# Performance work log

Hardware: AMD Instinct MI355X
Metric: run time of the kernel (lower is better)

Reference implementation:

```python
import jax, jax.numpy as jnp
import numpy as np

B, H, W = 4, 256, 256
TARGET_BETA0 = 5
TARGET_LIFETIME = 0.5
LOSS_SCALE = 100.0


def setup_inputs() -> dict:
    key = jax.random.key(0)
    k1, k2 = jax.random.split(key)
    prob_map = jax.random.uniform(k1, (B, 1, H, W), dtype=jnp.float32)
    roi_mask = (jax.random.uniform(k2, (B, 1, H, W)) < 0.9).astype(jnp.float32)
    return {"prob_map": prob_map, "roi_mask": roi_mask}


def _ph0_topk_loss(f):
    """0-dim persistent homology (V-filtration, 4-connectivity) of f:[H,W],
    then standard top-k MSE(target_lifetime) loss. Equivalent to
    cripser.compute_ph_torch(f, maxdim=0, filtration='V') + _standard_loss.
    Algorithm: Kruskal over grid edges with weight max(f[u],f[v]), elder rule.
    All combinatorics run on stop_gradient values; births/deaths are
    differentiable gathers from f at the paired pixel indices."""
    Hh, Ww = f.shape
    N = Hh * Ww
    fv = f.reshape(-1)
    fvc = jax.lax.stop_gradient(fv)

    idx2d = jnp.arange(N, dtype=jnp.int32).reshape(Hh, Ww)
    r_u = idx2d[:, :-1].reshape(-1)  # right edges
    r_v = r_u + 1
    d_u = idx2d[:-1, :].reshape(-1)  # down edges
    d_v = d_u + Ww
    eu = jnp.concatenate([r_u, d_u])
    ev = jnp.concatenate([r_v, d_v])
    ew = jnp.maximum(fvc[eu], fvc[ev])
    order = jnp.argsort(ew)  # process edges by increasing filtration value
    eu, ev = eu[order], ev[order]

    parent0 = jnp.arange(N, dtype=jnp.int32)

    def step(parent, uv):
        u, v = uv[0], uv[1]

        def find(x):
            return jax.lax.while_loop(lambda y: parent[y] != y, lambda y: parent[y], x)

        ru = find(u)
        rv = find(v)
        merge = ru != rv
        # Invariant: a root is the argmin pixel of its component, so
        # fvc[root] is the component's birth value. Elder rule: the root
        # with smaller birth value survives (ties -> smaller index).
        older_u = (fvc[ru] < fvc[rv]) | ((fvc[ru] == fvc[rv]) & (ru < rv))
        keep = jnp.where(older_u, ru, rv)
        die = jnp.where(older_u, rv, ru)
        b_idx = jnp.where(merge, die, -1)  # birth pixel of the dying comp
        d_pix = jnp.where(fvc[u] >= fvc[v], u, v)  # death = max endpoint
        d_idx = jnp.where(merge, d_pix, -1)
        parent = parent.at[die].set(jnp.where(merge, keep, die))
        parent = parent.at[u].set(jnp.where(merge, keep, ru))  # path compression
        parent = parent.at[v].set(jnp.where(merge, keep, rv))
        return parent, (b_idx, d_idx)

    _, (pb, pd_) = jax.lax.scan(step, parent0, jnp.stack([eu, ev], axis=1))

    valid = pb >= 0
    births = fv[jnp.maximum(pb, 0)]
    deaths = fv[jnp.maximum(pd_, 0)]
    life = jnp.where(valid, deaths - births, 0.0)  # lifetimes >= 0

    # sort descending; invalid slots to the end (keys are stop-gradient)
    key_ = jnp.where(valid, jax.lax.stop_gradient(life), -jnp.inf)
    top = jnp.argsort(-key_)[:TARGET_BETA0]
    topk = life[top]
    vk = valid[top]
    n_use = jnp.sum(vk)  # = min(num_finite, target_beta0)
    sq = jnp.where(vk, (topk - TARGET_LIFETIME) ** 2, 0.0)
    return jnp.sum(sq) / jnp.maximum(n_use, 1).astype(f.dtype)


def reference(prob_map, roi_mask):
    prob = prob_map[:, 0] * roi_mask[:, 0]  # roi masking; (1-roi)*0 is a no-op
    filtration = 1.0 - prob
    losses = jax.vmap(_ph0_topk_loss)(filtration)
    return jnp.mean(losses) * LOSS_SCALE
```

## Files before the change

### kernel.cpp

```cpp
#include <hip/hip_runtime.h>
#include <stdint.h>

#define NPIX 65536
#define NE   130560
#define NIMG 4
#define LTPB 1024
#define ETPB 1024
#define NBLK_L (NIMG*32)
#define TPIX 2048
#define EPAD 4096
#define KMAX 4096
#define HSZ  1024
#define LHSZ 2048
#define ECAP 4096
#define NCUT 2560
#define MTAILL 256
#define ETAIL  256
typedef unsigned long long u64;

__device__ __forceinline__ int ufind(unsigned* lbl, int x){
  int r = x, c = (int)lbl[r];
  while (c != r){ r = c; c = (int)lbl[r]; }
  while ((int)lbl[x] != r){ int n = (int)lbl[x]; lbl[x] = (unsigned)r; x = n; }
  return r;
}
__device__ __forceinline__ int ufind16(unsigned short* uf, int x){
  int r = x, c = (int)uf[r];
  while (c != r){ r = c; c = (int)uf[r]; }
  while ((int)uf[x] != r){ int n = (int)uf[x]; uf[x] = (unsigned short)r; x = n; }
  return r;
}

__device__ __forceinline__ void merge5(float* a, const float* b){
  float out[5]; int ia = 0, ib = 0;
  #pragma unroll
  for (int k = 0; k < 5; ++k){
    float av = (ia < 5) ? a[ia] : -2.0f;
    float bv = (ib < 5) ? b[ib] : -2.0f;
    if (av >= bv){ out[k] = av; ++ia; } else { out[k] = bv; ++ib; }
  }
  #pragma unroll
  for (int k = 0; k < 5; ++k) a[k] = out[k];
}

__device__ __forceinline__ void ins5(float* t5, float v){
  if (v > t5[4]){
    int j = 4;
    while (j > 0 && t5[j-1] < v){ t5[j] = t5[j-1]; --j; }
    t5[j] = v;
  }
}

__global__ __launch_bounds__(LTPB)
void ph0_local(const float* __restrict__ prob, const float* __restrict__ roi,
               float* __restrict__ LIFEg, unsigned* __restrict__ CIDg,
               u64* __restrict__ LAg,
               unsigned* __restrict__ C, unsigned* __restrict__ C2,
               unsigned* __restrict__ CUTWg, u64* __restrict__ RNKIg,
               float* __restrict__ T5g)
{
  const int blk = blockIdx.x;
  const int img = blk >> 5;
  const int tile = blk & 31;
  const int tr = tile >> 2, tc = tile & 3;
  const int gr0 = tr*32, gc0 = tc*64;
  const int tid = threadIdx.x;
  const int lane = tid & 63;

  const float* pm = prob + img*NPIX;
  const float* rm = roi  + img*NPIX;
  float* LIFE = LIFEg + img*NPIX;
  unsigned* CID = CIDg + img*NPIX;
  unsigned* CUTW = CUTWg + img*NCUT;
  u64* RNKI = RNKIg + (size_t)img*NPIX;
  u64* LA = LAg + (size_t)img*NE;

  __shared__ float          sf[TPIX];
  __shared__ unsigned       slbl[TPIX];
  __shared__ unsigned       smeb[2][TPIX];
  __shared__ float          slife[TPIX];
  __shared__ unsigned       blkm[TPIX];
  __shared__ unsigned short el[2][EPAD];
  __shared__ unsigned       aux[EPAD];
  __shared__ unsigned short fdl[2][EPAD];
  __shared__ unsigned       bkw[192];
  __shared__ unsigned short bkp[192];
  __shared__ unsigned       s_fired[TPIX/32];
  __shared__ float          s_t5w[(LTPB/64)*5];
  __shared__ int s_n[3];
  __shared__ int s_fd[2];

  float t5[5] = {-1.f,-1.f,-1.f,-1.f,-1.f};

  for (int p = tid; p < TPIX; p += LTPB){
    int gp = ((gr0 + (p>>6))<<8) + gc0 + (p&63);
    float fv = 1.0f - pm[gp]*rm[gp];
    sf[p] = fv; slbl[p] = (unsigned)p;
    smeb[0][p] = 0xFFFFFFFFu; smeb[1][p] = 0xFFFFFFFFu;
    blkm[p] = 0xFFFFFFFFu;
    slife[p] = 0.0f;
  }
  if (tid < 3) s_n[tid] = 0;
  if (tid < 2) s_fd[tid] = 0;
  if (tid < TPIX/32) s_fired[tid] = 0;
  for (int s = tid; s < 192; s += LTPB){
    unsigned wv = 0xFFFFFFFFu; int p = 0; int gq = -1;
    if (s < 32){ if (tc > 0){ p = s*64;        gq = ((gr0+s)<<8)    + gc0 - 1;  } }
    else if (s < 64){ int k=s-32;  if (tc < 3){ p = k*64+63;  gq = ((gr0+k)<<8)  + gc0 + 64; } }
    else if (s < 128){ int k=s-64; if (tr > 0){ p = k;        gq = ((gr0-1)<<8)  + gc0 + k;  } }
    else { int k=s-128;            if (tr < 7){ p = 31*64+k;  gq = ((gr0+32)<<8) + gc0 + k;  } }
    if (gq >= 0){
      int gp = ((gr0 + (p>>6))<<8) + gc0 + (p&63);
      float fp = 1.0f - pm[gp]*rm[gp];
      float fq = 1.0f - pm[gq]*rm[gq];
      wv = __float_as_uint(fmaxf(fp, fq));
    }
    bkw[s] = wv; bkp[s] = (unsigned short)p;
  }
  __syncthreads();

  if (tid < 192){
    int s = tid;
    if (s >= 32 && s < 64  && tc < 3) CUTW[(tc<<8) | (gr0 + (s-32))] = bkw[s];
    if (s >= 128           && tr < 7) CUTW[768 + (tr<<8) + (gc0 + (s-128))] = bkw[s];
    if (bkw[s] != 0xFFFFFFFFu) atomicMin(&blkm[(int)bkp[s]], bkw[s]);
  }

  int M = EPAD, cur = 0, rd = 0;
  bool tailm = false;
  for (; rd < 100000; ++rd){
    int nxt = cur ^ 1;
    unsigned* sme  = smeb[rd & 1];
    unsigned* smeN = smeb[(rd+1) & 1];
    {
      int pv = (rd & 1) ^ 1;
      int fc = s_fd[pv];
      for (int i = tid; i < fc; i += LTPB){
        int d = (int)fdl[pv][i];
        atomicMin(&blkm[ufind(slbl, d)], blkm[d]);
      }
    }
    int Mpad = (M + 63) & ~63;
    for (int idx = tid; idx < Mpad; idx += LTPB){
      bool keep = false; int e=0,u=0,v=0,a=0,b=0;
      if (idx < M){
        e = (rd == 0) ? idx : (int)el[cur][idx];
        bool valid;
        if (e < 2048){ u=e; v=e+1; valid = ((e&63)!=63); }
        else { u=e-2048; v=u+64; valid = ((u>>6)!=31); }
        if (valid){
          a = ufind(slbl,u); b = ufind(slbl,v);
          if (a != b){
            unsigned wb = __float_as_uint(fmaxf(sf[u],sf[v]));
            atomicMin(&sme[a],wb); atomicMin(&sme[b],wb);
            keep = true;
          }
        }
      }
      u64 m = __ballot(keep);
      if (m){
        int pos0 = __popcll(m & ((1ULL<<lane)-1));
        int leader = __ffsll((long long)m)-1;
        int base = 0;
        if (lane == leader) base = atomicAdd(&s_n[rd%3], __popcll(m));
        base = __shfl(base, leader);
        if (keep){
          el[nxt][base+pos0] = (unsigned short)e;
          aux[base+pos0] = (unsigned)a | ((unsigned)b<<16);
        }
      }
    }
    __syncthreads();
    int n = s_n[rd%3];
    cur = nxt;
    if (n == M || n == 0){ M = n; break; }
    M = n;
    for (int idx = tid; idx < M; idx += LTPB){
      int e = (int)el[cur][idx];
      unsigned ab = aux[idx];
      int a = (int)(ab & 0xFFFFu), b = (int)(ab >> 16);
      int u, v;
      if (e < 2048){ u = e; v = e + 1; } else { u = e - 2048; v = u + 64; }
      float w = fmaxf(sf[u], sf[v]);
      unsigned wb = __float_as_uint(w);
      float fa = sf[a], fb = sf[b];
      bool bd = (fb < fa) || ((fb == fa) && (b < a));
      int die = bd ? a : b, keep = bd ? b : a;
      bool fire = false;
      if (sme[die] == wb && blkm[die] >= wb){
        fire = true;
        slbl[die] = (unsigned)keep;
        float lt = w - (bd ? fa : fb);
        slife[die] = lt;
        atomicMin(&blkm[keep], blkm[die]);
        unsigned bbit = 1u << (die & 31);
        if (!(atomicOr(&s_fired[die >> 5], bbit) & bbit)) ins5(t5, lt);
      }
      smeN[a] = 0xFFFFFFFFu; smeN[b] = 0xFFFFFFFFu;
      u64 fm = __ballot(fire);
      if (fm){
        int pos0 = __popcll(fm & ((1ULL<<lane)-1));
        int leader = __ffsll((long long)fm)-1;
        int base2 = 0;
        if (lane == leader) base2 = atomicAdd(&s_fd[rd&1], __popcll(fm));
        base2 = __shfl(base2, leader);
        if (fire) fdl[rd&1][base2+pos0] = (unsigned short)die;
      }
    }
    if (tid == 0){ s_n[(rd+1)%3] = 0; s_fd[(rd&1)^1] = 0; }
    __syncthreads();
    if (M <= MTAILL){ ++rd; tailm = true; break; }
  }

  if (tailm){
    if (tid < 64){
      for (;; ++rd){
        unsigned* sme  = smeb[rd & 1];
        unsigned* smeN = smeb[(rd+1) & 1];
        {
          int pv = (rd & 1) ^ 1;
          int fc = s_fd[pv];
          for (int i = lane; i < fc; i += 64){
            int d = (int)fdl[pv][i];
            atomicMin(&blkm[ufind(slbl, d)], blkm[d]);
          }
        }
        __builtin_amdgcn_wave_barrier();
        int nxt = cur ^ 1;
        int nacc = 0;
        for (int i0 = 0; i0 < M; i0 += 64){
          int idx = i0 + lane;
          bool keep = false; int e = 0, a = 0, b = 0;
          if (idx < M){
            e = (int)el[cur][idx];
            int u, v;
            if (e < 2048){ u = e; v = e + 1; } else { u = e - 2048; v = u + 64; }
            a = ufind(slbl,u); b = ufind(slbl,v);
            if (a != b){
              unsigned wb = __float_as_uint(fmaxf(sf[u],sf[v]));
              atomicMin(&sme[a],wb); atomicMin(&sme[b],wb);
              keep = true;
            }
          }
          u64 mm = __ballot(keep);
          if (keep){
            int pos = nacc + __popcll(mm & ((1ULL<<lane)-1));
            el[nxt][pos] = (unsigned short)e;
            aux[pos] = (unsigned)a | ((unsigned)b<<16);
          }
          nacc += __popcll(mm);
        }
        __builtin_amdgcn_wave_barrier();
        int n = nacc;
        cur = nxt;
        if (n == M || n == 0){ M = n; break; }
        M = n;
        int fdc = 0;
        for (int i0 = 0; i0 < M; i0 += 64){
          int idx = i0 + lane;
          bool fire = false; int die = 0;
          if (idx < M){
            int e = (int)el[cur][idx];
            unsigned ab = aux[idx];
            int a = (int)(ab & 0xFFFFu), b = (int)(ab >> 16);
            int u, v;
            if (e < 2048){ u = e; v = e + 1; } else { u = e - 2048; v = u + 64; }
            float w = fmaxf(sf[u], sf[v]);
            unsigned wb = __float_as_uint(w);
            float fa = sf[a], fb = sf[b];
            bool bd = (fb < fa) || ((fb == fa) && (b < a));
            die = bd ? a : b;
            int kp = bd ? b : a;
            if (sme[die] == wb && blkm[die] >= wb){
              fire = true;
              slbl[die] = (unsigned)kp;
              float lt = w - (bd ? fa : fb);
              slife[die] = lt;
              atomicMin(&blkm[kp], blkm[die]);
              unsigned bbit = 1u << (die & 31);
              if (!(atomicOr(&s_fired[die >> 5], bbit) & bbit)) ins5(t5, lt);
            }
            smeN[a] = 0xFFFFFFFFu; smeN[b] = 0xFFFFFFFFu;
          }
          u64 fm = __ballot(fire);
          if (fire){
            int pos = fdc + __popcll(fm & ((1ULL<<lane)-1));
            fdl[rd&1][pos] = (unsigned short)die;
          }
          fdc += __popcll(fm);
        }
        if (lane == 0){ s_fd[rd&1] = fdc; s_fd[(rd&1)^1] = 0; }
        __builtin_amdgcn_wave_barrier();
      }
      if (lane == 0){ s_n[0] = M; s_n[1] = cur; }
    }
    __syncthreads();
    M = s_n[0]; cur = s_n[1];
  }

  unsigned* posm = smeb[0];
  for (int p = tid; p < TPIX; p += LTPB){
    if ((int)slbl[p] == p){
      unsigned pos = atomicAdd(&C2[img], 1u);
      posm[p] = pos;
      unsigned gp = (unsigned)(((gr0 + (p>>6))<<8) + gc0 + (p&63));
      RNKI[pos] = ((u64)__float_as_uint(sf[p]) << 32) | gp;
    }
  }
  __syncthreads();
  for (int p = tid; p < TPIX; p += LTPB){
    int r = ufind(slbl, p);
    int gp = ((gr0 + (p>>6))<<8) + gc0 + (p&63);
    CID[gp] = posm[r];
    LIFE[gp] = slife[p];
  }
  __syncthreads();

  unsigned* hk = (unsigned*)&el[cur ^ 1][0];
  unsigned* hw = slbl;
  for (int i = tid; i < LHSZ; i += LTPB){ hk[i] = 0xFFFFFFFFu; hw[i] = 0xFFFFFFFFu; }
  __syncthreads();

  unsigned* ctr = &C[img];
  int Mpad2 = (M + 63) & ~63;
  for (int idx = tid; idx < Mpad2; idx += LTPB){
    bool spill = false;
    u64 rec = 0;
    if (idx < M){
      int e = (int)el[cur][idx];
      unsigned ab = aux[idx];
      int a = (int)(ab & 0xFFFFu), b = (int)(ab >> 16);
      int u, v;
      if (e < 2048){ u = e; v = e + 1; } else { u = e - 2048; v = u + 64; }
      unsigned wb = __float_as_uint(fmaxf(sf[u], sf[v]));
      int lo = a < b ? a : b, hi = a < b ? b : a;
      unsigned key = ((unsigned)lo << 11) | (unsigned)hi;
      unsigned h = ((key * 2654435761u) >> 21) & (LHSZ-1);
      bool ins = false;
      #pragma unroll
      for (int t = 0; t < 8; ++t){
        unsigned old = atomicCAS(&hk[h], 0xFFFFFFFFu, key);
        if (old == 0xFFFFFFFFu || old == key){ atomicMin(&hw[h], wb); ins = true; break; }
        h = (h + 1) & (LHSZ-1);
      }
      if (!ins){
        spill = true;
        rec = ((u64)wb << 32) | ((u64)posm[a] << 16) | posm[b];
      }
    }
    u64 m = __ballot(spill);
    if (m){
      int pos0 = __popcll(m & ((1ULL<<lane)-1));
      int leader = __ffsll((long long)m)-1;
      unsigned base = 0;
      if (lane == leader) base = atomicAdd(ctr, (unsigned)__popcll(m));
      base = (unsigned)__shfl((int)base, leader);
      if (spill) LA[base + pos0] = rec;
    }
  }
  __syncthreads();
  for (int h = tid; h < LHSZ; h += LTPB){
    unsigned key = hk[h];
    bool ok = (key != 0xFFFFFFFFu);
    u64 rec = 0;
    if (ok){
      int a = (int)(key >> 11), b = (int)(key & 0x7FFu);
      rec = ((u64)hw[h] << 32) | ((u64)posm[a] << 16) | posm[b];
    }
    u64 m = __ballot(ok);
    if (m){
      int pos0 = __popcll(m & ((1ULL<<lane)-1));
      int leader = __ffsll((long long)m)-1;
      unsigned base = 0;
      if (lane == leader) base = atomicAdd(ctr, (unsigned)__popcll(m));
      base = (unsigned)__shfl((int)base, leader);
      if (ok) LA[base + pos0] = rec;
    }
  }

  #pragma unroll
  for (int off = 1; off < 64; off <<= 1){
    float o[5];
    #pragma unroll
    for (int k = 0; k < 5; ++k) o[k] = __shfl_xor(t5[k], off);
    merge5(t5, o);
  }
  if (lane == 0){
    int wv = tid >> 6;
    #pragma unroll
    for (int k = 0; k < 5; ++k) s_t5w[wv*5+k] = t5[k];
  }
  __syncthreads();
  if (tid < 64){
    float u5[5];
    #pragma unroll
    for (int k = 0; k < 5; ++k) u5[k] = (tid < LTPB/64) ? s_t5w[tid*5+k] : -2.0f;
    #pragma unroll
    for (int off = 1; off < 16; off <<= 1){
      float o[5];
      #pragma unroll
      for (int k = 0; k < 5; ++k) o[k] = __shfl_xor(u5[k], off);
      merge5(u5, o);
    }
    if (tid == 0){
      #pragma unroll
      for (int k = 0; k < 5; ++k) T5g[blk*5+k] = u5[k];
    }
  }
}

#define RUN_ROUNDS_GLOBAL(UF, ME, RNK)                                       \
  for (int k = tid; k < K; k += ETPB) UF[k] = (unsigned short)k;             \
  __syncthreads();                                                           \
  for (int rdg = 0; rdg < 70000 && n > 0; ++rdg){                            \
    for (int k = tid; k < K; k += ETPB) ME[k] = 0xFFFFFFFFu;                 \
    if (tid == 0) s_n[0] = 0;                                                \
    __syncthreads();                                                         \
    int Mpad = (n + 63) & ~63;                                               \
    for (int idx = tid; idx < Mpad; idx += ETPB){                            \
      bool keep = false; unsigned wb = 0; int a = 0, b = 0;                  \
      if (idx < n){                                                          \
        u64 rec = src[idx];                                                  \
        wb = (unsigned)(rec >> 32);                                          \
        a = (int)((rec >> 16) & 0xFFFFu);                                    \
        b = (int)(rec & 0xFFFFu);                                            \
        a = ufind16(UF, a); b = ufind16(UF, b);                              \
        if (a != b){ atomicMin(&ME[a], wb); atomicMin(&ME[b], wb); keep = true; } \
      }                                                                      \
      u64 m = __ballot(keep);                                                \
      if (m){                                                                \
        int pos0 = __popcll(m & ((1ULL<<lane)-1));                           \
        int leader = __ffsll((long long)m)-1;                                \
        int base = 0;                                                        \
        if (lane == leader) base = atomicAdd(&s_n[0], __popcll(m));          \
        base = __shfl(base, leader);                                         \
        if (keep) dst[base+pos0] = ((u64)wb<<32)|((u64)(unsigned)a<<16)|(unsigned)b; \
      }                                                                      \
    }                                                                        \
    __syncthreads();                                                         \
    int nn = s_n[0];                                                         \
    for (int idx = tid; idx < nn; idx += ETPB){                              \
      u64 rec = dst[idx];                                                    \
      unsigned wb = (unsigned)(rec >> 32);                                   \
      int a = (int)((rec >> 16) & 0xFFFFu);                                  \
      int b = (int)(rec & 0xFFFFu);                                          \
      bool bd = RNK[b] < RNK[a];                                             \
      int die = bd ? a : b, kp = bd ? b : a;                                 \
      if (ME[die] == wb){                                                    \
        UF[die] = (unsigned short)kp;                                        \
        u64 rk = RNK[die];                                                   \
        life[(unsigned)(rk & 0xFFFFFFFFu)] =                                 \
            __uint_as_float(wb) - __uint_as_float((unsigned)(rk >> 32));     \
      }                                                                      \
    }                                                                        \
    __syncthreads();                                                         \
    u64* t = src; src = dst; dst = t; n = nn;                                \
  }

__global__ __launch_bounds__(ETPB)
void ph0_endgame(float* __restrict__ LIFEg, unsigned* __restrict__ CIDg,
                 const unsigned* __restrict__ CUTWg, u64* __restrict__ RNKIg,
                 u64* __restrict__ LAg, u64* __restrict__ LBg,
                 const unsigned* __restrict__ C, const unsigned* __restrict__ C2,
                 const float* __restrict__ T5g,
                 float* __restrict__ LOSS, unsigned* __restrict__ DONE,
                 float* __restrict__ out)
{
  const int img = blockIdx.x, tid = threadIdx.x;
  const int lane = tid & 63;
  float* life = LIFEg + img*NPIX;
  unsigned* cid = CIDg + img*NPIX;
  const unsigned* cw = CUTWg + img*NCUT;
  u64* RNKI = RNKIg + (size_t)img*NPIX;
  u64* src = LAg + (size_t)img*NE;
  u64* dst = LBg + (size_t)img*NE;

  __shared__ unsigned short s_uf[KMAX];
  __shared__ unsigned s_meB[2*KMAX];
  __shared__ unsigned s_hkB[2*HSZ];
  __shared__ unsigned s_hwB[2*HSZ];
  __shared__ u64 s_rnk[KMAX];
  __shared__ u64 s_lstA[ECAP];
  __shared__ u64 s_lstB[ECAP];
  __shared__ unsigned s_fired[KMAX/32];
  __shared__ float s_w5[(ETPB/64)*5];
  __shared__ int s_n[3];

  const int K = (int)C2[img];
  const int nInt = (int)C[img];

  for (int s = tid; s < NCUT; s += ETPB){
    int gu, gv;
    if (s < 768){ int ci = s >> 8, row = s & 255, col = 63 + (ci<<6); gu = (row<<8)+col; gv = gu+1; }
    else { int k = s - 768; int ri = k >> 8, colh = k & 255, gr = 31 + (ri<<5); gu = (gr<<8)+colh; gv = gu+256; }
    unsigned ia = cid[gu];
    unsigned ib = cid[gv];
    unsigned wb = cw[s];
    s_lstA[s] = ((u64)wb << 32) | ((u64)ia << 16) | ib;
  }
  if (tid < 3) s_n[tid] = 0;
  int n = nInt + NCUT;

  float t5[5] = {-1.f,-1.f,-1.f,-1.f,-1.f};

  if (K <= KMAX){
    for (int k = tid; k < K; k += ETPB){
      s_uf[k] = (unsigned short)k;
      s_rnk[k] = RNKI[k];
      s_meB[k] = 0xFFFFFFFFu;
    }
    for (int h = tid; h < HSZ; h += ETPB){ s_hkB[h] = 0xFFFFFFFFu; s_hwB[h] = 0xFFFFFFFFu; }
    if (tid < KMAX/32) s_fired[tid] = 0;
    if (tid < 32*5) ins5(t5, T5g[img*(32*5) + tid]);
    __syncthreads();

    u64 *lsrc = s_lstA, *ldst = s_lstB;
    int rd = 0; bool tailm = false;

    for (; rd < 70000; ++rd){
      const int bi = rd & 1;
      unsigned* me  = s_meB + bi*KMAX;
      unsigned* meN = s_meB + (bi^1)*KMAX;
      unsigned* hk = s_hkB + bi*HSZ;
      unsigned* hw = s_hwB + bi*HSZ;
      const bool useHash = (n > 1024);
      int Mpad = (n + 63) & ~63;
      for (int idx = tid; idx < Mpad; idx += ETPB){
        bool app = false; unsigned wb = 0; int a = 0, b = 0;
        if (idx < n){
          u64 rec;
          if (rd == 0) rec = (idx < NCUT) ? lsrc[idx] : src[idx - NCUT];
          else         rec = (idx < ECAP) ? lsrc[idx] : src[idx];
          a = (int)((rec >> 16) & 0xFFFFu);
          b = (int)(rec & 0xFFFFu);
          a = ufind16(s_uf, a); b = ufind16(s_uf, b);
          if (a != b){
            wb = (unsigned)(rec >> 32);
            if (useHash){
              int lo = a < b ? a : b, hi = a < b ? b : a;
              unsigned key = ((unsigned)lo << 12) | (unsigned)hi;
              unsigned h = ((key * 2654435761u) >> 20) & (HSZ-1);
              bool ins = false;
              #pragma unroll
              for (int t = 0; t < 8; ++t){
                unsigned old = atomicCAS(&hk[h], 0xFFFFFFFFu, key);
                if (old == 0xFFFFFFFFu || old == key){ atomicMin(&hw[h], wb); ins = true; break; }
                h = (h + 1) & (HSZ-1);
              }
              if (!ins){ atomicMin(&me[a], wb); atomicMin(&me[b], wb); app = true; }
            } else {
              atomicMin(&me[a], wb); atomicMin(&me[b], wb); app = true;
            }
          }
        }
        u64 m = __ballot(app);
        if (m){
          int pos0 = __popcll(m & ((1ULL<<lane)-1));
          int leader = __ffsll((long long)m)-1;
          int base = 0;
          if (lane == leader) base = atomicAdd(&s_n[rd%3], __popcll(m));
          base = __shfl(base, leader);
          if (app){
            u64 r = ((u64)wb<<32)|((u64)(unsigned)a<<16)|(unsigned)b;
            int pos = base+pos0;
            if (pos < ECAP) ldst[pos] = r; else dst[pos] = r;
          }
        }
      }
      __syncthreads();
      if (useHash){
        for (int h = tid; h < HSZ; h += ETPB){
          unsigned key = hk[h];
          bool okk = (key != 0xFFFFFFFFu);
          unsigned wb = 0; int a = 0, b = 0;
          if (okk){
            a = (int)(key >> 12); b = (int)(key & 0xFFFu);
            wb = hw[h];
            atomicMin(&me[a], wb); atomicMin(&me[b], wb);
          }
          u64 m = __ballot(okk);
          if (m){
            int pos0 = __popcll(m & ((1ULL<<lane)-1));
            int leader = __ffsll((long long)m)-1;
            int base = 0;
            if (lane == leader) base = atomicAdd(&s_n[rd%3], __popcll(m));
            base = __shfl(base, leader);
            if (okk){
              u64 r = ((u64)wb<<32)|((u64)(unsigned)a<<16)|(unsigned)b;
              int pos = base+pos0;
              if (pos < ECAP) ldst[pos] = r; else dst[pos] = r;
            }
          }
        }
        __syncthreads();
      }
      int nn = s_n[rd%3];
      if (nn == 0) break;
      for (int idx = tid; idx < nn; idx += ETPB){
        u64 rec = (idx < ECAP) ? ldst[idx] : dst[idx];
        unsigned wb = (unsigned)(rec >> 32);
        int a = (int)((rec >> 16) & 0xFFFFu);
        int b = (int)(rec & 0xFFFFu);
        u64 ra = s_rnk[a], rb = s_rnk[b];
        bool bd = rb < ra;
        int die = bd ? a : b, kp = bd ? b : a;
        if (me[die] == wb){
          s_uf[die] = (unsigned short)kp;
          unsigned bbit = 1u << (die & 31);
          if (!(atomicOr(&s_fired[die >> 5], bbit) & bbit)){
            u64 rk = bd ? ra : rb;
            ins5(t5, __uint_as_float(wb) - __uint_as_float((unsigned)(rk >> 32)));
          }
        }
        meN[a] = 0xFFFFFFFFu; meN[b] = 0xFFFFFFFFu;
      }
      if (nn > 1024){
        unsigned* hkN = s_hkB + (bi^1)*HSZ;
        unsigned* hwN = s_hwB + (bi^1)*HSZ;
        for (int h = tid; h < HSZ; h += ETPB){ hkN[h] = 0xFFFFFFFFu; hwN[h] = 0xFFFFFFFFu; }
      }
      if (tid == 0) s_n[(rd+1)%3] = 0;
      __syncthreads();
      { u64* t = src; src = dst; dst = t; }
      { u64* t2 = lsrc; lsrc = ldst; ldst = t2; }
      n = nn;
      if (n <= ETAIL){ ++rd; tailm = true; break; }
    }

    if (tailm){
      if (tid < 64){
        for (;; ++rd){
          const int bi = rd & 1;
          unsigned* me  = s_meB + bi*KMAX;
          unsigned* meN = s_meB + (bi^1)*KMAX;
          int nacc = 0;
          for (int i0 = 0; i0 < n; i0 += 64){
            int idx = i0 + lane;
            bool app = false; unsigned wb = 0; int a = 0, b = 0;
            if (idx < n){
              u64 rec = lsrc[idx];
              a = (int)((rec >> 16) & 0xFFFFu);
              b = (int)(rec & 0xFFFFu);
              a = ufind16(s_uf, a); b = ufind16(s_uf, b);
              if (a != b){
                wb = (unsigned)(rec >> 32);
                atomicMin(&me[a], wb); atomicMin(&me[b], wb);
                app = true;
              }
            }
            u64 mm = __ballot(app);
            if (app){
              int pos = nacc + __popcll(mm & ((1ULL<<lane)-1));
              ldst[pos] = ((u64)wb<<32)|((u64)(unsigned)a<<16)|(unsigned)b;
            }
            nacc += __popcll(mm);
          }
          __builtin_amdgcn_wave_barrier();
          int nn = nacc;
          if (nn == 0) break;
          for (int i0 = 0; i0 < nn; i0 += 64){
            int idx = i0 + lane;
            if (idx < nn){
              u64 rec = ldst[idx];
              unsigned wb = (unsigned)(rec >> 32);
              int a = (int)((rec >> 16) & 0xFFFFu);
              int b = (int)(rec & 0xFFFFu);
              u64 ra = s_rnk[a], rb = s_rnk[b];
              bool bd = rb < ra;
              int die = bd ? a : b, kp = bd ? b : a;
              if (me[die] == wb){
                s_uf[die] = (unsigned short)kp;
                unsigned bbit = 1u << (die & 31);
                if (!(atomicOr(&s_fired[die >> 5], bbit) & bbit)){
                  u64 rk = bd ? ra : rb;
                  ins5(t5, __uint_as_float(wb) - __uint_as_float((unsigned)(rk >> 32)));
                }
              }
              meN[a] = 0xFFFFFFFFu; meN[b] = 0xFFFFFFFFu;
            }
          }
          __builtin_amdgcn_wave_barrier();
          { u64* t2 = lsrc; lsrc = ldst; ldst = t2; }
          n = nn;
        }
      }
      __syncthreads();
    }
  } else {
    __syncthreads();
    for (int s = tid; s < NCUT; s += ETPB) src[nInt + s] = s_lstA[s];
    __syncthreads();
    unsigned short* g_uf = (unsigned short*)cid;
    unsigned*       g_me = (unsigned*)(cid + NPIX/2);
    u64*            g_rnk = RNKI;
    RUN_ROUNDS_GLOBAL(g_uf, g_me, g_rnk)
    for (int i = tid; i < NPIX; i += ETPB) ins5(t5, life[i]);
  }

  #pragma unroll
  for (int off = 1; off < 64; off <<= 1){
    float o[5];
    #pragma unroll
    for (int k = 0; k < 5; ++k) o[k] = __shfl_xor(t5[k], off);
    merge5(t5, o);
  }
  if (lane == 0){
    int wv = tid >> 6;
    #pragma unroll
    for (int k = 0; k < 5; ++k) s_w5[wv*5+k] = t5[k];
  }
  __syncthreads();
  if (tid < 64){
    float u5[5];
    #pragma unroll
    for (int k = 0; k < 5; ++k) u5[k] = (tid < ETPB/64) ? s_w5[tid*5+k] : -2.0f;
    #pragma unroll
    for (int off = 1; off < 16; off <<= 1){
      float o[5];
      #pragma unroll
      for (int k = 0; k < 5; ++k) o[k] = __shfl_xor(u5[k], off);
      merge5(u5, o);
    }
    if (tid == 0){
      float lsum = 0.0f;
      #pragma unroll
      for (int k = 0; k < 5; ++k){ float d = u5[k] - 0.5f; lsum += d*d; }
      atomicExch(&LOSS[img], lsum * 0.2f);
      __threadfence();
      unsigned prev = atomicAdd(DONE, 1u);
      if (prev == NIMG - 1){
        float s = 0.0f;
        #pragma unroll
        for (int i = 0; i < NIMG; ++i) s += atomicAdd(&LOSS[i], 0.0f);
        out[0] = s * 25.0f;
      }
    }
  }
}

extern "C" void kernel_launch(void* const* d_in, const int* in_sizes, int n_in,
                              void* d_out, int out_size, void* d_ws, size_t ws_size,
                              hipStream_t stream)
{
  const float* prob = (const float*)d_in[0];
  const float* roi  = (const float*)d_in[1];
  char* ws = (char*)d_ws;
  const size_t SZL = (size_t)4*NE*8;
  float*    LIFE = (float*)(ws + (1u<<20));
  unsigned* CID  = (unsigned*)(ws + (2u<<20));
  unsigned* CUTW = (unsigned*)(ws + (3u<<20));
  u64*      LA   = (u64*)(ws + (5u<<20));
  u64*      LB   = (u64*)(ws + (5u<<20) + SZL);
  u64*      RNKI = (u64*)(ws + (5u<<20) + 2*SZL);
  unsigned* C    = (unsigned*)(ws + (5u<<20) + 2*SZL + (2u<<20));
  unsigned* C2   = C + 4;
  unsigned* DONE = C + 8;
  float*    LOSS = (float*)((char*)C + 64);
  float*    T5   = (float*)(ws + (5u<<20) + 2*SZL - 2560);
  float*    out  = (float*)d_out;

  hipMemsetAsync(C, 0, 64, stream);
  ph0_local<<<NBLK_L, LTPB, 0, stream>>>(prob, roi, LIFE, CID, LA, C, C2, CUTW, RNKI, T5);
  ph0_endgame<<<NIMG, ETPB, 0, stream>>>(LIFE, CID, CUTW, RNKI, LA, LB, C, C2, T5, LOSS, DONE, out);
}
```

Baseline: 263.0 us.

## Replace Boruvka tail rounds with bitonic-sorted Kruskal sweep using per-wave claims

```diff
diff --git a/kernel.cpp b/kernel.cpp
--- a/kernel.cpp
+++ b/kernel.cpp
@@ -14,8 +14,9 @@
 #define LHSZ 2048
 #define ECAP 4096
 #define NCUT 2560
-#define MTAILL 256
-#define ETAIL  256
+#define MTAILL 512
+#define ETAIL  512
+#define RCAPL 40
 typedef unsigned long long u64;
 
 __device__ __forceinline__ int ufind(unsigned* lbl, int x){
@@ -209,93 +210,102 @@
     }
     if (tid == 0){ s_n[(rd+1)%3] = 0; s_fd[(rd&1)^1] = 0; }
     __syncthreads();
-    if (M <= MTAILL){ ++rd; tailm = true; break; }
+    if (M <= MTAILL || rd >= RCAPL){ ++rd; tailm = true; break; }
   }
 
   if (tailm){
+    {
+      int pv = (rd & 1) ^ 1;
+      int fc = s_fd[pv];
+      for (int i = tid; i < fc; i += LTPB){
+        int d = (int)fdl[pv][i];
+        atomicMin(&blkm[ufind(slbl, d)], blkm[d]);
+      }
+    }
+    int P = 1; while (P < M) P <<= 1;
+    unsigned* skey = aux;
+    unsigned short* sval = el[cur];
+    unsigned* claim = smeb[0];
+    for (int i = tid; i < P; i += LTPB){
+      if (i < M){
+        int e = (int)sval[i];
+        int u, v;
+        if (e < 2048){ u = e; v = e + 1; } else { u = e - 2048; v = u + 64; }
+        skey[i] = __float_as_uint(fmaxf(sf[u], sf[v]));
+      } else skey[i] = 0xFFFFFFFFu;
+    }
+    for (int i = tid; i < TPIX; i += LTPB) claim[i] = 0xFFFFFFFFu;
+    __syncthreads();
+    for (int k = 2; k <= P; k <<= 1){
+      for (int j = k >> 1; j > 0; j >>= 1){
+        for (int i = tid; i < P; i += LTPB){
+          int l = i ^ j;
+          if (l > i){
+            unsigned ki = skey[i], kl = skey[l];
+            if ((ki > kl) == ((i & k) == 0)){
+              skey[i] = kl; skey[l] = ki;
+              unsigned short tv = sval[i]; sval[i] = sval[l]; sval[l] = tv;
+            }
+          }
+        }
+        __syncthreads();
+      }
+    }
     if (tid < 64){
-      for (;; ++rd){
-        unsigned* sme  = smeb[rd & 1];
-        unsigned* smeN = smeb[(rd+1) & 1];
-        {
-          int pv = (rd & 1) ^ 1;
-          int fc = s_fd[pv];
-          for (int i = lane; i < fc; i += 64){
-            int d = (int)fdl[pv][i];
-            atomicMin(&blkm[ufind(slbl, d)], blkm[d]);
-          }
-        }
-        __builtin_amdgcn_wave_barrier();
-        int nxt = cur ^ 1;
-        int nacc = 0;
-        for (int i0 = 0; i0 < M; i0 += 64){
-          int idx = i0 + lane;
-          bool keep = false; int e = 0, a = 0, b = 0;
-          if (idx < M){
-            e = (int)el[cur][idx];
-            int u, v;
-            if (e < 2048){ u = e; v = e + 1; } else { u = e - 2048; v = u + 64; }
-            a = ufind(slbl,u); b = ufind(slbl,v);
-            if (a != b){
-              unsigned wb = __float_as_uint(fmaxf(sf[u],sf[v]));
-              atomicMin(&sme[a],wb); atomicMin(&sme[b],wb);
-              keep = true;
-            }
-          }
-          u64 mm = __ballot(keep);
-          if (keep){
-            int pos = nacc + __popcll(mm & ((1ULL<<lane)-1));
-            el[nxt][pos] = (unsigned short)e;
-            aux[pos] = (unsigned)a | ((unsigned)b<<16);
-          }
-          nacc += __popcll(mm);
-        }
-        __builtin_amdgcn_wave_barrier();
-        int n = nacc;
-        cur = nxt;
-        if (n == M || n == 0){ M = n; break; }
-        M = n;
-        int fdc = 0;
-        for (int i0 = 0; i0 < M; i0 += 64){
-          int idx = i0 + lane;
-          bool fire = false; int die = 0;
-          if (idx < M){
-            int e = (int)el[cur][idx];
-            unsigned ab = aux[idx];
-            int a = (int)(ab & 0xFFFFu), b = (int)(ab >> 16);
-            int u, v;
-            if (e < 2048){ u = e; v = e + 1; } else { u = e - 2048; v = u + 64; }
-            float w = fmaxf(sf[u], sf[v]);
-            unsigned wb = __float_as_uint(w);
+      int survM = 0;
+      for (int base = 0; base < M; base += 64){
+        int rank = base + lane;
+        bool live = (rank < M), surv = false;
+        int e = 0, u = 0, v = 0; unsigned wb = 0;
+        if (live){
+          e = (int)sval[rank];
+          if (e < 2048){ u = e; v = e + 1; } else { u = e - 2048; v = u + 64; }
+          wb = skey[rank];
+        }
+        for (int si = 0; si < 8192; ++si){
+          if (!__ballot(live)) break;
+          int a = 0, b = 0; bool cl = false;
+          if (live){
+            a = ufind(slbl, u); b = ufind(slbl, v);
+            if (a == b) live = false;
+            else { atomicMin(&claim[a], (unsigned)rank);
+                   atomicMin(&claim[b], (unsigned)rank); cl = true; }
+          }
+          __builtin_amdgcn_wave_barrier();
+          if (live && cl && claim[a] == (unsigned)rank && claim[b] == (unsigned)rank){
             float fa = sf[a], fb = sf[b];
             bool bd = (fb < fa) || ((fb == fa) && (b < a));
-            die = bd ? a : b;
-            int kp = bd ? b : a;
-            if (sme[die] == wb && blkm[die] >= wb){
-              fire = true;
+            int die = bd ? a : b, kp = bd ? b : a;
+            if (blkm[die] < wb){
+              surv = true;
+              atomicMin(&blkm[a], wb);
+              atomicMin(&blkm[b], wb);
+            } else {
               slbl[die] = (unsigned)kp;
-              float lt = w - (bd ? fa : fb);
+              atomicMin(&blkm[kp], blkm[die]);
+              float lt = __uint_as_float(wb) - (bd ? fa : fb);
               slife[die] = lt;
-              atomicMin(&blkm[kp], blkm[die]);
               unsigned bbit = 1u << (die & 31);
               if (!(atomicOr(&s_fired[die >> 5], bbit) & bbit)) ins5(t5, lt);
             }
-            smeN[a] = 0xFFFFFFFFu; smeN[b] = 0xFFFFFFFFu;
-          }
-          u64 fm = __ballot(fire);
-          if (fire){
-            int pos = fdc + __popcll(fm & ((1ULL<<lane)-1));
-            fdl[rd&1][pos] = (unsigned short)die;
-          }
-          fdc += __popcll(fm);
-        }
-        if (lane == 0){ s_fd[rd&1] = fdc; s_fd[(rd&1)^1] = 0; }
-        __builtin_amdgcn_wave_barrier();
-      }
-      if (lane == 0){ s_n[0] = M; s_n[1] = cur; }
+            live = false;
+          }
+          __builtin_amdgcn_wave_barrier();
+          if (cl){ claim[a] = 0xFFFFFFFFu; claim[b] = 0xFFFFFFFFu; }
+          __builtin_amdgcn_wave_barrier();
+        }
+        u64 sm = __ballot(surv);
+        if (surv){
+          int pos = survM + __popcll(sm & ((1ULL << lane) - 1));
+          el[cur ^ 1][pos] = (unsigned short)e;
+        }
+        survM += __popcll(sm);
+      }
+      if (lane == 0) s_n[0] = survM;
     }
     __syncthreads();
-    M = s_n[0]; cur = s_n[1];
+    M = s_n[0];
+    cur ^= 1;
   }
 
   unsigned* posm = smeb[0];
@@ -313,6 +323,13 @@
     int gp = ((gr0 + (p>>6))<<8) + gc0 + (p&63);
     CID[gp] = posm[r];
     LIFE[gp] = slife[p];
+  }
+  __syncthreads();
+  for (int idx = tid; idx < M; idx += LTPB){
+    int e = (int)el[cur][idx];
+    int u, v;
+    if (e < 2048){ u = e; v = e + 1; } else { u = e - 2048; v = u + 64; }
+    aux[idx] = (unsigned)ufind(slbl, u) | ((unsigned)ufind(slbl, v) << 16);
   }
   __syncthreads();
 
@@ -332,20 +349,22 @@
       int a = (int)(ab & 0xFFFFu), b = (int)(ab >> 16);
       int u, v;
       if (e < 2048){ u = e; v = e + 1; } else { u = e - 2048; v = u + 64; }
-      unsigned wb = __float_as_uint(fmaxf(sf[u], sf[v]));
-      int lo = a < b ? a : b, hi = a < b ? b : a;
-      unsigned key = ((unsigned)lo << 11) | (unsigned)hi;
-      unsigned h = ((key * 2654435761u) >> 21) & (LHSZ-1);
-      bool ins = false;
-      #pragma unroll
-      for (int t = 0; t < 8; ++t){
-        unsigned old = atomicCAS(&hk[h], 0xFFFFFFFFu, key);
-        if (old == 0xFFFFFFFFu || old == key){ atomicMin(&hw[h], wb); ins = true; break; }
-        h = (h + 1) & (LHSZ-1);
-      }
-      if (!ins){
-        spill = true;
-        rec = ((u64)wb << 32) | ((u64)posm[a] << 16) | posm[b];
+      if (a != b){
+        unsigned wb = __float_as_uint(fmaxf(sf[u], sf[v]));
+        int lo = a < b ? a : b, hi = a < b ? b : a;
+        unsigned key = ((unsigned)lo << 11) | (unsigned)hi;
+        unsigned h = ((key * 2654435761u) >> 21) & (LHSZ-1);
+        bool ins = false;
+        #pragma unroll
+        for (int t = 0; t < 8; ++t){
+          unsigned old = atomicCAS(&hk[h], 0xFFFFFFFFu, key);
+          if (old == 0xFFFFFFFFu || old == key){ atomicMin(&hw[h], wb); ins = true; break; }
+          h = (h + 1) & (LHSZ-1);
+        }
+        if (!ins){
+          spill = true;
+          rec = ((u64)wb << 32) | ((u64)posm[a] << 16) | posm[b];
+        }
       }
     }
     u64 m = __ballot(spill);
@@ -624,64 +643,64 @@
       { u64* t = src; src = dst; dst = t; }
       { u64* t2 = lsrc; lsrc = ldst; ldst = t2; }
       n = nn;
-      if (n <= ETAIL){ ++rd; tailm = true; break; }
+      if (n <= ETAIL || (rd >= RCAPL && n <= ECAP)){ ++rd; tailm = true; break; }
     }
 
     if (tailm){
+      int P = 1; while (P < n) P <<= 1;
+      unsigned* claim = s_meB;
+      for (int i = tid; i < P; i += ETPB) if (i >= n) lsrc[i] = ~0ULL;
+      for (int i = tid; i < KMAX; i += ETPB) claim[i] = 0xFFFFFFFFu;
+      __syncthreads();
+      for (int k2 = 2; k2 <= P; k2 <<= 1){
+        for (int j = k2 >> 1; j > 0; j >>= 1){
+          for (int i = tid; i < P; i += ETPB){
+            int l = i ^ j;
+            if (l > i){
+              u64 ki = lsrc[i], kl = lsrc[l];
+              if ((ki > kl) == ((i & k2) == 0)){ lsrc[i] = kl; lsrc[l] = ki; }
+            }
+          }
+          __syncthreads();
+        }
+      }
       if (tid < 64){
-        for (;; ++rd){
-          const int bi = rd & 1;
-          unsigned* me  = s_meB + bi*KMAX;
-          unsigned* meN = s_meB + (bi^1)*KMAX;
-          int nacc = 0;
-          for (int i0 = 0; i0 < n; i0 += 64){
-            int idx = i0 + lane;
-            bool app = false; unsigned wb = 0; int a = 0, b = 0;
-            if (idx < n){
-              u64 rec = lsrc[idx];
-              a = (int)((rec >> 16) & 0xFFFFu);
-              b = (int)(rec & 0xFFFFu);
-              a = ufind16(s_uf, a); b = ufind16(s_uf, b);
-              if (a != b){
-                wb = (unsigned)(rec >> 32);
-                atomicMin(&me[a], wb); atomicMin(&me[b], wb);
-                app = true;
+        for (int base = 0; base < n; base += 64){
+          int rank = base + lane;
+          bool live = (rank < n);
+          int a0 = 0, b0 = 0; unsigned wb = 0;
+          if (live){
+            u64 rec = lsrc[rank];
+            wb = (unsigned)(rec >> 32);
+            a0 = (int)((rec >> 16) & 0xFFFFu);
+            b0 = (int)(rec & 0xFFFFu);
+          }
+          for (int si = 0; si < 8192; ++si){
+            if (!__ballot(live)) break;
+            int die = 0, kp = 0; bool cl = false; u64 rkd = 0;
+            if (live){
+              int a = ufind16(s_uf, a0), b = ufind16(s_uf, b0);
+              if (a == b) live = false;
+              else {
+                u64 ra = s_rnk[a], rb = s_rnk[b];
+                bool bd = rb < ra;
+                die = bd ? a : b; kp = bd ? b : a; rkd = bd ? ra : rb;
+                atomicMin(&claim[die], (unsigned)rank);
+                cl = true;
               }
             }
-            u64 mm = __ballot(app);
-            if (app){
-              int pos = nacc + __popcll(mm & ((1ULL<<lane)-1));
-              ldst[pos] = ((u64)wb<<32)|((u64)(unsigned)a<<16)|(unsigned)b;
+            __builtin_amdgcn_wave_barrier();
+            if (live && cl && claim[die] == (unsigned)rank){
+              s_uf[die] = (unsigned short)kp;
+              unsigned bbit = 1u << (die & 31);
+              if (!(atomicOr(&s_fired[die >> 5], bbit) & bbit))
+                ins5(t5, __uint_as_float(wb) - __uint_as_float((unsigned)(rkd >> 32)));
+              live = false;
             }
-            nacc += __popcll(mm);
-          }
-          __builtin_amdgcn_wave_barrier();
-          int nn = nacc;
-          if (nn == 0) break;
-          for (int i0 = 0; i0 < nn; i0 += 64){
-            int idx = i0 + lane;
-            if (idx < nn){
-              u64 rec = ldst[idx];
-              unsigned wb = (unsigned)(rec >> 32);
-              int a = (int)((rec >> 16) & 0xFFFFu);
-              int b = (int)(rec & 0xFFFFu);
-              u64 ra = s_rnk[a], rb = s_rnk[b];
-              bool bd = rb < ra;
-              int die = bd ? a : b, kp = bd ? b : a;
-              if (me[die] == wb){
-                s_uf[die] = (unsigned short)kp;
-                unsigned bbit = 1u << (die & 31);
-                if (!(atomicOr(&s_fired[die >> 5], bbit) & bbit)){
-                  u64 rk = bd ? ra : rb;
-                  ins5(t5, __uint_as_float(wb) - __uint_as_float((unsigned)(rk >> 32)));
-                }
-              }
-              meN[a] = 0xFFFFFFFFu; meN[b] = 0xFFFFFFFFu;
-            }
-          }
-          __builtin_amdgcn_wave_barrier();
-          { u64* t2 = lsrc; lsrc = ldst; ldst = t2; }
-          n = nn;
+            __builtin_amdgcn_wave_barrier();
+            if (cl) claim[die] = 0xFFFFFFFFu;
+            __builtin_amdgcn_wave_barrier();
+          }
         }
       }
       __syncthreads();
```

New measurement: 383.7 us. 1.46x slower.
